# Performance work log

Measured on AMD Instinct MI355X. Metric: run time of the kernel, lower is better.

## Reference

```python
import jax, jax.numpy as jnp
import numpy as np

EMB = 256
N = 262144
B = 512
SLOPE = 0.01  # torch LeakyReLU default negative slope


def leaky_relu(x):
    return jnp.where(x >= 0, x, SLOPE * x)


def setup_inputs() -> dict:
    key = jax.random.key(0)
    ks = jax.random.split(key, 10)
    s = 1.0 / np.sqrt(EMB)
    s2 = 1.0 / np.sqrt(2 * EMB)
    return {
        "xg_prev": jax.random.normal(ks[0], (B, EMB), jnp.float32),
        "x": jax.random.normal(ks[1], (N, EMB), jnp.float32),
        "batch_ind": jnp.sort(jax.random.randint(ks[2], (N,), 0, B)),
        "W_mask": jax.random.uniform(ks[3], (EMB, 1), jnp.float32, -s, s),
        "b_mask": jax.random.uniform(ks[4], (1,), jnp.float32, -s, s),
        "W_feat": jax.random.uniform(ks[5], (EMB, EMB), jnp.float32, -s, s),
        "b_feat": jax.random.uniform(ks[6], (EMB,), jnp.float32, -s, s),
        "W_t": jax.random.uniform(ks[7], (2 * EMB, EMB), jnp.float32, -s2, s2),
        "b_t": jax.random.uniform(ks[8], (EMB,), jnp.float32, -s2, s2),
    }


def reference(xg_prev, x, batch_ind, W_mask, b_mask, W_feat, b_feat, W_t, b_t):
    # GlobalAttention pooling (PyG): gate = att_mask(x), feat = att_feat(x)
    gate = (x @ W_mask + b_mask)[:, 0]                      # [N]
    feat = leaky_relu(x @ W_feat + b_feat)                  # [N, EMB]
    # segment-wise stable softmax over gate per graph
    seg_max = jax.ops.segment_max(gate, batch_ind, num_segments=B)  # [B]
    seg_max = jnp.where(jnp.isfinite(seg_max), seg_max, 0.0)
    e = jnp.exp(gate - seg_max[batch_ind])                  # [N]
    denom = jax.ops.segment_sum(e, batch_ind, num_segments=B)      # [B]
    w = e / jnp.maximum(denom[batch_ind], 1e-16)            # [N]
    xg = jax.ops.segment_sum(w[:, None] * feat, batch_ind, num_segments=B)  # [B, EMB]
    # concat -> linear -> leaky_relu -> residual
    h = jnp.concatenate([xg, xg_prev], axis=1)              # [B, 2*EMB]
    out = leaky_relu(h @ W_t + b_t) + xg_prev               # [B, EMB]
    return out
```

## Files before the change

### kernel.cpp

```cpp
#include <hip/hip_runtime.h>
#include <cstdint>
#include <cstddef>

#define NROWS 262144
#define EMB 256
#define NB 512
#define NCOPY 8
#define SLOPE 0.01f

typedef __attribute__((ext_vector_type(8))) short short8;
typedef __attribute__((ext_vector_type(4))) float f32x4;

__device__ __forceinline__ unsigned short f2bf(float f) {
    unsigned u = __float_as_uint(f);
    u += 0x7FFFu + ((u >> 16) & 1u);
    return (unsigned short)(u >> 16);
}

__device__ __forceinline__ short8 pack8(const float4& lo, const float4& hi) {
    short8 s;
    s[0] = (short)f2bf(lo.x); s[1] = (short)f2bf(lo.y);
    s[2] = (short)f2bf(lo.z); s[3] = (short)f2bf(lo.w);
    s[4] = (short)f2bf(hi.x); s[5] = (short)f2bf(hi.y);
    s[6] = (short)f2bf(hi.z); s[7] = (short)f2bf(hi.w);
    return s;
}

__device__ __forceinline__ void gld16f(float* l, const float* g) {
    __builtin_amdgcn_global_load_lds(
        (const __attribute__((address_space(1))) unsigned int*)g,
        (__attribute__((address_space(3))) unsigned int*)l, 16, 0, 0);
}
__device__ __forceinline__ void gld16u(unsigned short* l, const unsigned short* g) {
    __builtin_amdgcn_global_load_lds(
        (const __attribute__((address_space(1))) unsigned int*)g,
        (__attribute__((address_space(3))) unsigned int*)l, 16, 0, 0);
}

__global__ __launch_bounds__(256) void k_init(float4* xgPart4, float4* dPart4) {
    int i = blockIdx.x * 256 + threadIdx.x;
    if (i < NCOPY * NB * EMB / 4) xgPart4[i] = (float4){0.f, 0.f, 0.f, 0.f};
    else dPart4[i - NCOPY * NB * EMB / 4] = (float4){0.f, 0.f, 0.f, 0.f};
}

__global__ __launch_bounds__(256) void k_prep(const float* __restrict__ Wf,
                                              unsigned short* __restrict__ Wt2) {
    int b = blockIdx.x, t = threadIdx.x;
    float v = Wf[(size_t)b * EMB + t];
    Wt2[((size_t)(b >> 3) << 11) + (t << 3) + (b & 7)] = f2bf(v);
}

#define STAGE(B, KT) do {                                                         \
    _Pragma("unroll")                                                             \
    for (int q = 0; q < 2; q++) {                                                 \
        const int i_ = q * 512 + t;                                               \
        const int row_ = i_ >> 3, c_ = i_ & 7;                                    \
        const int cs_ = c_ ^ (row_ & 7);                                          \
        gld16f(&xbuf[B][i_ * 4], x + ((r0 + row_) << 8) + (KT) + (cs_ << 2));     \
    }                                                                             \
    _Pragma("unroll")                                                             \
    for (int q = 0; q < 2; q++) {                                                 \
        const int i_ = q * 512 + t;                                               \
        const int slab_ = i_ >> 8, off_ = i_ & 255;                               \
        gld16u(&bbuf[B][slab_ * 2048 + off_ * 8],                                 \
               Wt2 + (((size_t)((KT) >> 3) + slab_) << 11) + off_ * 8);           \
    }                                                                             \
} while (0)

__global__ __launch_bounds__(512, 4) void k_fused(const float* __restrict__ x,
                                                  const unsigned short* __restrict__ Wt2,
                                                  const float* __restrict__ wm,
                                                  const float* __restrict__ bfeat,
                                                  const int* __restrict__ bind,
                                                  float* __restrict__ dPart,
                                                  float* __restrict__ xgPart) {
    __shared__ float          xbuf[2][128 * 32];
    __shared__ unsigned short bbuf[2][32 * 256];
    __shared__ float wm_s[256];
    __shared__ float w_s[128];
    __shared__ float pxg[2][256];
    __shared__ float pden[2];
    __shared__ int   seg_s[128];
    __shared__ int   segid_s[8];
    __shared__ int   uni_s[8];

    const int t    = threadIdx.x;
    const int lane = t & 63;
    const int w    = t >> 6;
    const int wr   = w >> 1, wc = w & 1;
    const int fr   = lane & 15;
    const int fg   = lane >> 4;
    const size_t r0 = (size_t)blockIdx.x * 128;
    const int cp   = blockIdx.x & (NCOPY - 1);

    if (t < 256) { wm_s[t] = wm[t]; pxg[0][t] = 0.f; pxg[1][t] = 0.f; }
    if (t < 128) seg_s[t] = bind[r0 + t];
    if (t < 2)   pden[t] = 0.f;

    STAGE(0, 0);

    f32x4 acc[2][8];
#pragma unroll
    for (int m = 0; m < 2; m++)
#pragma unroll
        for (int n = 0; n < 8; n++) acc[m][n] = (f32x4){0.f, 0.f, 0.f, 0.f};
    float gp0 = 0.f, gp1 = 0.f;

#pragma unroll
    for (int s = 0; s < 8; s++) {
        const int buf = s & 1;
        if (s < 7) STAGE(buf ^ 1, (s + 1) * 32);
        if (s < 7) asm volatile("s_waitcnt vmcnt(4)" ::: "memory");
        else       asm volatile("s_waitcnt vmcnt(0)" ::: "memory");
        __builtin_amdgcn_sched_barrier(0);
        __builtin_amdgcn_s_barrier();
        __builtin_amdgcn_sched_barrier(0);

        const float* xb = &xbuf[buf][0];
        const unsigned short* bb = &bbuf[buf][0];

        const float4 wa  = *reinterpret_cast<const float4*>(&wm_s[s * 32 + fg * 8]);
        const float4 wbv = *reinterpret_cast<const float4*>(&wm_s[s * 32 + fg * 8 + 4]);
        short8 a0, a1;
        {
            const int r  = wr * 32 + fr;
            const int sl = (fg * 2) ^ (r & 7);
            const float4 lo = *reinterpret_cast<const float4*>(&xb[r * 32 + sl * 4]);
            const float4 hi = *reinterpret_cast<const float4*>(&xb[r * 32 + (sl ^ 1) * 4]);
            gp0 += lo.x * wa.x + lo.y * wa.y + lo.z * wa.z + lo.w * wa.w
                 + hi.x * wbv.x + hi.y * wbv.y + hi.z * wbv.z + hi.w * wbv.w;
            a0 = pack8(lo, hi);
        }
        {
            const int r  = wr * 32 + 16 + fr;
            const int sl = (fg * 2) ^ (r & 7);
            const float4 lo = *reinterpret_cast<const float4*>(&xb[r * 32 + sl * 4]);
            const float4 hi = *reinterpret_cast<const float4*>(&xb[r * 32 + (sl ^ 1) * 4]);
            gp1 += lo.x * wa.x + lo.y * wa.y + lo.z * wa.z + lo.w * wa.w
                 + hi.x * wbv.x + hi.y * wbv.y + hi.z * wbv.z + hi.w * wbv.w;
            a1 = pack8(lo, hi);
        }
#pragma unroll
        for (int n = 0; n < 8; n++) {
            const short8 b = *reinterpret_cast<const short8*>(
                &bb[fg * 2048 + ((wc * 128 + n * 16 + fr) << 3)]);
            acc[0][n] = __builtin_amdgcn_mfma_f32_16x16x32_bf16(a0, b, acc[0][n], 0, 0, 0);
            acc[1][n] = __builtin_amdgcn_mfma_f32_16x16x32_bf16(a1, b, acc[1][n], 0, 0, 0);
        }

        asm volatile("s_waitcnt lgkmcnt(0)" ::: "memory");
        __builtin_amdgcn_sched_barrier(0);
        __builtin_amdgcn_s_barrier();
        __builtin_amdgcn_sched_barrier(0);
    }

    gp0 += __shfl_xor(gp0, 16, 64); gp0 += __shfl_xor(gp0, 32, 64);
    gp1 += __shfl_xor(gp1, 16, 64); gp1 += __shfl_xor(gp1, 32, 64);
    if (wc == 0 && lane < 16) {
        w_s[wr * 32 + lane]      = expf(gp0);
        w_s[wr * 32 + 16 + lane] = expf(gp1);
    }
    if (t < 8) {
        int s0 = seg_s[t * 16], ok = 1;
#pragma unroll
        for (int i = 1; i < 16; i++) ok &= (seg_s[t * 16 + i] == s0);
        segid_s[t] = s0;
        uni_s[t]   = ok;
    }
    __syncthreads();

    const int sid0 = seg_s[0];
    const int sid1 = seg_s[127];

    if (t < 8) {
        if (uni_s[t]) {
            float s = 0.f;
#pragma unroll
            for (int i = 0; i < 16; i++) s += w_s[t * 16 + i];
            const int sid = segid_s[t];
            if (sid == sid0)      atomicAdd(&pden[0], s);
            else if (sid == sid1) atomicAdd(&pden[1], s);
            else atomicAdd(&dPart[cp * NB + sid], s);
        } else {
            for (int i = 0; i < 16; i++) {
                const int sd = seg_s[t * 16 + i];
                const float e = w_s[t * 16 + i];
                if (sd == sid0)      atomicAdd(&pden[0], e);
                else if (sd == sid1) atomicAdd(&pden[1], e);
                else atomicAdd(&dPart[cp * NB + sd], e);
            }
        }
    }

#pragma unroll
    for (int m = 0; m < 2; m++) {
        const int g    = wr * 2 + m;
        const int uni  = uni_s[g];
        const int sid  = segid_s[g];
        const int rowb = wr * 32 + m * 16;
#pragma unroll
        for (int n = 0; n < 8; n++) {
            const int col = wc * 128 + n * 16 + fr;
            const float bia = bfeat[col];
            float vr[4];
#pragma unroll
            for (int r = 0; r < 4; r++) {
                const int row = rowb + fg * 4 + r;
                float v = acc[m][n][r] + bia;
                v = (v >= 0.f) ? v : SLOPE * v;
                vr[r] = v * w_s[row];
            }
            if (uni) {
                float s = vr[0] + vr[1] + vr[2] + vr[3];
                s += __shfl_xor(s, 16, 64);
                s += __shfl_xor(s, 32, 64);
                if (fg == 0) {
                    if (sid == sid0)      atomicAdd(&pxg[0][col], s);
                    else if (sid == sid1) atomicAdd(&pxg[1][col], s);
                    else atomicAdd(&xgPart[((size_t)(cp * NB + sid) << 8) + col], s);
                }
            } else {
#pragma unroll
                for (int r = 0; r < 4; r++) {
                    const int sd = seg_s[rowb + fg * 4 + r];
                    if (sd == sid0)      atomicAdd(&pxg[0][col], vr[r]);
                    else if (sd == sid1) atomicAdd(&pxg[1][col], vr[r]);
                    else atomicAdd(&xgPart[((size_t)(cp * NB + sd) << 8) + col], vr[r]);
                }
            }
        }
    }
    __syncthreads();

    if (t < 256) {
        atomicAdd(&xgPart[((size_t)(cp * NB + sid0) << 8) + t], pxg[0][t]);
    } else if (sid1 != sid0) {
        atomicAdd(&xgPart[((size_t)(cp * NB + sid1) << 8) + (t - 256)], pxg[1][t - 256]);
    }
    if (t == 0) atomicAdd(&dPart[cp * NB + sid0], pden[0]);
    if (t == 1 && sid1 != sid0) atomicAdd(&dPart[cp * NB + sid1], pden[1]);
}

__global__ __launch_bounds__(256) void k_out(const float* __restrict__ xgPart,
                                             const float* __restrict__ dPart,
                                             const float* __restrict__ xgp,
                                             const float* __restrict__ Wtr,
                                             const float* __restrict__ bt,
                                             float* __restrict__ out) {
    __shared__ float h[8][512];
    const int c  = threadIdx.x;
    const int b0 = blockIdx.x * 8;
#pragma unroll
    for (int r = 0; r < 8; r++) {
        const int b = b0 + r;
        float den = 0.f, s = 0.f;
#pragma unroll
        for (int cpy = 0; cpy < NCOPY; cpy++) {
            den += dPart[cpy * NB + b];
            s   += xgPart[((size_t)(cpy * NB + b) << 8) + c];
        }
        h[r][c]       = s / fmaxf(den, 1e-16f);
        h[r][EMB + c] = xgp[(size_t)b * EMB + c];
    }
    __syncthreads();
    float acc[8] = {0.f, 0.f, 0.f, 0.f, 0.f, 0.f, 0.f, 0.f};
    for (int k = 0; k < 2 * EMB; k++) {
        float wv = Wtr[(size_t)k * EMB + c];
#pragma unroll
        for (int r = 0; r < 8; r++) acc[r] += h[r][k] * wv;
    }
#pragma unroll
    for (int r = 0; r < 8; r++) {
        float v = acc[r] + bt[c];
        v = (v >= 0.f) ? v : SLOPE * v;
        out[(size_t)(b0 + r) * EMB + c] = v + xgp[(size_t)(b0 + r) * EMB + c];
    }
}

extern "C" void kernel_launch(void* const* d_in, const int* in_sizes, int n_in,
                              void* d_out, int out_size, void* d_ws, size_t ws_size,
                              hipStream_t stream) {
    const float* xgp  = (const float*)d_in[0];
    const float* x    = (const float*)d_in[1];
    const int*   bind = (const int*)d_in[2];
    const float* Wm   = (const float*)d_in[3];
    const float* Wf   = (const float*)d_in[5];
    const float* bf   = (const float*)d_in[6];
    const float* Wtr  = (const float*)d_in[7];
    const float* bt   = (const float*)d_in[8];
    float* out = (float*)d_out;

    char* ws = (char*)d_ws;
    unsigned short* Wt2    = (unsigned short*)ws;
    float*          dPart  = (float*)(ws + 131072);
    float*          xgPart = (float*)(ws + 131072 + 16384);

    hipLaunchKernelGGL(k_init,  dim3(1028),        dim3(256), 0, stream,
                       (float4*)xgPart, (float4*)dPart);
    hipLaunchKernelGGL(k_prep,  dim3(256),         dim3(256), 0, stream, Wf, Wt2);
    hipLaunchKernelGGL(k_fused, dim3(NROWS / 128), dim3(512), 0, stream,
                       x, Wt2, Wm, bf, bind, dPart, xgPart);
    hipLaunchKernelGGL(k_out,   dim3(NB / 8),      dim3(256), 0, stream,
                       xgPart, dPart, xgp, Wtr, bt, out);
}
```

Measured before the change: 142.6 us.

## Merge init into prep kernel and spread output GEMM over one block per graph

```diff
diff --git a/kernel.cpp b/kernel.cpp
--- a/kernel.cpp
+++ b/kernel.cpp
@@ -37,17 +37,19 @@
         (__attribute__((address_space(3))) unsigned int*)l, 16, 0, 0);
 }
 
-__global__ __launch_bounds__(256) void k_init(float4* xgPart4, float4* dPart4) {
-    int i = blockIdx.x * 256 + threadIdx.x;
-    if (i < NCOPY * NB * EMB / 4) xgPart4[i] = (float4){0.f, 0.f, 0.f, 0.f};
-    else dPart4[i - NCOPY * NB * EMB / 4] = (float4){0.f, 0.f, 0.f, 0.f};
-}
-
 __global__ __launch_bounds__(256) void k_prep(const float* __restrict__ Wf,
-                                              unsigned short* __restrict__ Wt2) {
-    int b = blockIdx.x, t = threadIdx.x;
-    float v = Wf[(size_t)b * EMB + t];
-    Wt2[((size_t)(b >> 3) << 11) + (t << 3) + (b & 7)] = f2bf(v);
+                                              unsigned short* __restrict__ Wt2,
+                                              float4* __restrict__ xgPart4,
+                                              float4* __restrict__ dPart4) {
+    const int b = blockIdx.x, t = threadIdx.x;
+    if (b < 256) {
+        float v = Wf[(size_t)b * EMB + t];
+        Wt2[((size_t)(b >> 3) << 11) + (t << 3) + (b & 7)] = f2bf(v);
+    } else {
+        const int i = (b - 256) * 256 + t;
+        if (i < NCOPY * NB * EMB / 4) xgPart4[i] = (float4){0.f, 0.f, 0.f, 0.f};
+        else dPart4[i - NCOPY * NB * EMB / 4] = (float4){0.f, 0.f, 0.f, 0.f};
+    }
 }
 
 #define STAGE(B, KT) do {                                                         \
@@ -110,8 +112,9 @@
     for (int s = 0; s < 8; s++) {
         const int buf = s & 1;
         if (s < 7) STAGE(buf ^ 1, (s + 1) * 32);
-        if (s < 7) asm volatile("s_waitcnt vmcnt(4)" ::: "memory");
-        else       asm volatile("s_waitcnt vmcnt(0)" ::: "memory");
+        if (s == 0)     asm volatile("s_waitcnt vmcnt(4) lgkmcnt(0)" ::: "memory");
+        else if (s < 7) asm volatile("s_waitcnt vmcnt(4)" ::: "memory");
+        else            asm volatile("s_waitcnt vmcnt(0)" ::: "memory");
         __builtin_amdgcn_sched_barrier(0);
         __builtin_amdgcn_s_barrier();
         __builtin_amdgcn_sched_barrier(0);
@@ -204,11 +207,11 @@
             const float bia = bfeat[col];
             float vr[4];
 #pragma unroll
-            for (int r = 0; r < 4; r++) {
-                const int row = rowb + fg * 4 + r;
-                float v = acc[m][n][r] + bia;
+            for (int r2 = 0; r2 < 4; r2++) {
+                const int row = rowb + fg * 4 + r2;
+                float v = acc[m][n][r2] + bia;
                 v = (v >= 0.f) ? v : SLOPE * v;
-                vr[r] = v * w_s[row];
+                vr[r2] = v * w_s[row];
             }
             if (uni) {
                 float s = vr[0] + vr[1] + vr[2] + vr[3];
@@ -221,11 +224,11 @@
                 }
             } else {
 #pragma unroll
-                for (int r = 0; r < 4; r++) {
-                    const int sd = seg_s[rowb + fg * 4 + r];
-                    if (sd == sid0)      atomicAdd(&pxg[0][col], vr[r]);
-                    else if (sd == sid1) atomicAdd(&pxg[1][col], vr[r]);
-                    else atomicAdd(&xgPart[((size_t)(cp * NB + sd) << 8) + col], vr[r]);
+                for (int r2 = 0; r2 < 4; r2++) {
+                    const int sd = seg_s[rowb + fg * 4 + r2];
+                    if (sd == sid0)      atomicAdd(&pxg[0][col], vr[r2]);
+                    else if (sd == sid1) atomicAdd(&pxg[1][col], vr[r2]);
+                    else atomicAdd(&xgPart[((size_t)(cp * NB + sd) << 8) + col], vr[r2]);
                 }
             }
         }
@@ -247,34 +250,29 @@
                                              const float* __restrict__ Wtr,
                                              const float* __restrict__ bt,
                                              float* __restrict__ out) {
-    __shared__ float h[8][512];
-    const int c  = threadIdx.x;
-    const int b0 = blockIdx.x * 8;
-#pragma unroll
-    for (int r = 0; r < 8; r++) {
-        const int b = b0 + r;
-        float den = 0.f, s = 0.f;
-#pragma unroll
-        for (int cpy = 0; cpy < NCOPY; cpy++) {
-            den += dPart[cpy * NB + b];
-            s   += xgPart[((size_t)(cpy * NB + b) << 8) + c];
-        }
-        h[r][c]       = s / fmaxf(den, 1e-16f);
-        h[r][EMB + c] = xgp[(size_t)b * EMB + c];
-    }
+    __shared__ float h[512];
+    const int c = threadIdx.x;
+    const int b = blockIdx.x;
+
+    float den = 0.f, s = 0.f;
+#pragma unroll
+    for (int cpy = 0; cpy < NCOPY; cpy++) {
+        den += dPart[cpy * NB + b];
+        s   += xgPart[((size_t)(cpy * NB + b) << 8) + c];
+    }
+    const float xp = xgp[(size_t)b * EMB + c];
+    h[c]       = s / fmaxf(den, 1e-16f);
+    h[EMB + c] = xp;
     __syncthreads();
-    float acc[8] = {0.f, 0.f, 0.f, 0.f, 0.f, 0.f, 0.f, 0.f};
+
+    float acc = 0.f;
+#pragma unroll 8
     for (int k = 0; k < 2 * EMB; k++) {
-        float wv = Wtr[(size_t)k * EMB + c];
-#pragma unroll
-        for (int r = 0; r < 8; r++) acc[r] += h[r][k] * wv;
-    }
-#pragma unroll
-    for (int r = 0; r < 8; r++) {
-        float v = acc[r] + bt[c];
-        v = (v >= 0.f) ? v : SLOPE * v;
-        out[(size_t)(b0 + r) * EMB + c] = v + xgp[(size_t)(b0 + r) * EMB + c];
-    }
+        acc += h[k] * Wtr[(size_t)k * EMB + c];
+    }
+    float v = acc + bt[c];
+    v = (v >= 0.f) ? v : SLOPE * v;
+    out[(size_t)b * EMB + c] = v + xp;
 }
 
 extern "C" void kernel_launch(void* const* d_in, const int* in_sizes, int n_in,
@@ -295,11 +293,10 @@
     float*          dPart  = (float*)(ws + 131072);
     float*          xgPart = (float*)(ws + 131072 + 16384);
 
-    hipLaunchKernelGGL(k_init,  dim3(1028),        dim3(256), 0, stream,
-                       (float4*)xgPart, (float4*)dPart);
-    hipLaunchKernelGGL(k_prep,  dim3(256),         dim3(256), 0, stream, Wf, Wt2);
+    hipLaunchKernelGGL(k_prep,  dim3(256 + 1028),  dim3(256), 0, stream,
+                       Wf, Wt2, (float4*)xgPart, (float4*)dPart);
     hipLaunchKernelGGL(k_fused, dim3(NROWS / 128), dim3(512), 0, stream,
                        x, Wt2, Wm, bf, bind, dPart, xgPart);
-    hipLaunchKernelGGL(k_out,   dim3(NB / 8),      dim3(256), 0, stream,
+    hipLaunchKernelGGL(k_out,   dim3(NB),          dim3(256), 0, stream,
                        xgPart, dPart, xgp, Wtr, bt, out);
 }
```

Measured after the change: 136.3 us. 1.05x faster.
